# Optimization experiments

Hardware: AMD Instinct MI355X
Metric: run time of the kernel (lower is better)

The kernel has to match this reference:

```python
import jax, jax.numpy as jnp
import numpy as np

B, T, C = 4, 2048, 2048
N_HEAD = 16
HEAD_DIM = C // N_HEAD
ROPE_BASE = 10000.0


def setup_inputs() -> dict:
    key = jax.random.key(0)
    k1, k2, k3 = jax.random.split(key, 3)
    x = jax.random.normal(k1, (B, T, C), dtype=jnp.float32)
    w_attn = jax.random.normal(k2, (3 * C, C), dtype=jnp.float32) * (1.0 / np.sqrt(C))
    w_proj = jax.random.normal(k3, (C, C), dtype=jnp.float32) * (1.0 / np.sqrt(C))
    return {"x": x, "w_attn": w_attn, "w_proj": w_proj}


def _apply_rope(x, cos, sin):
    # x: [B, H, T, hd]; interleaved pairs (even, odd) rotated
    x_ = x.reshape(*x.shape[:-1], -1, 2)
    x0, x1 = x_[..., 0], x_[..., 1]
    x0r = x0 * cos - x1 * sin
    x1r = x0 * sin + x1 * cos
    return jnp.stack([x0r, x1r], axis=-1).reshape(x.shape)


def reference(x, w_attn, w_proj):
    Bx, Tx, Cx = x.shape
    hd = Cx // N_HEAD
    d = hd // 2

    qkv = jnp.einsum('btc,fc->btf', x, w_attn)  # [B,T,3C]
    q, k, v = jnp.split(qkv, 3, axis=-1)

    def to_heads(t):
        return t.reshape(Bx, Tx, N_HEAD, hd).transpose(0, 2, 1, 3)  # [B,H,T,hd]

    q, k, v = to_heads(q), to_heads(k), to_heads(v)

    # RoPE
    theta = 1.0 / (ROPE_BASE ** (2.0 * jnp.arange(d, dtype=jnp.float32) / hd))
    t = jnp.arange(Tx, dtype=x.dtype)
    freqs = jnp.outer(t, theta.astype(x.dtype))  # [T, d]
    cos = jnp.cos(freqs)[None, None]  # [1,1,T,d]
    sin = jnp.sin(freqs)[None, None]
    q = _apply_rope(q, cos, sin)
    k = _apply_rope(k, cos, sin)

    # Causal attention
    scale = 1.0 / jnp.sqrt(jnp.asarray(hd, dtype=x.dtype))
    scores = jnp.einsum('bhqd,bhkd->bhqk', q, k) * scale
    causal = jnp.tril(jnp.ones((Tx, Tx), dtype=bool))
    scores = jnp.where(causal[None, None], scores, jnp.asarray(-jnp.inf, dtype=scores.dtype))
    attn = jax.nn.softmax(scores, axis=-1)
    y = jnp.einsum('bhqk,bhkd->bhqd', attn, v)  # [B,H,T,hd]

    y = y.transpose(0, 2, 1, 3).reshape(Bx, Tx, Cx)
    return jnp.einsum('btc,oc->bto', y, w_proj)
```

## Files before the change

kernel.cpp:

```cpp
#include <hip/hip_runtime.h>

#define B_ 4
#define T_ 2048
#define C_ 2048
#define H_ 16
#define N1_ 6144
#define M_ 8192
#define SCALE_ 0.08838834764831845f

typedef unsigned short u16;
typedef __bf16 bf16x8 __attribute__((ext_vector_type(8)));
typedef float f32x4 __attribute__((ext_vector_type(4)));
typedef float f32x16 __attribute__((ext_vector_type(16)));

__device__ __forceinline__ u16 f2bf(float f) {
  union { float f; unsigned u; } v; v.f = f;
  return (u16)((v.u + 0x7fffu + ((v.u >> 16) & 1u)) >> 16);
}
__device__ __forceinline__ float bf2f(u16 h) {
  union { unsigned u; float f; } v; v.u = ((unsigned)h) << 16;
  return v.f;
}

__device__ __forceinline__ void gld16(const void* g, void* l) {
  __builtin_amdgcn_global_load_lds(
      (__attribute__((address_space(1))) unsigned int*)(unsigned long long)g,
      (__attribute__((address_space(3))) unsigned int*)(unsigned)(unsigned long long)l,
      16, 0, 0);
}

__global__ void k_cast(const float* __restrict__ in, u16* __restrict__ out, int n4) {
  int i = blockIdx.x * 256 + threadIdx.x;
  if (i >= n4) return;
  float4 v = reinterpret_cast<const float4*>(in)[i];
  ushort4 o;
  o.x = f2bf(v.x); o.y = f2bf(v.y); o.z = f2bf(v.z); o.w = f2bf(v.w);
  reinterpret_cast<ushort4*>(out)[i] = o;
}

__global__ void k_trig(float2* __restrict__ trig) {
  int idx = blockIdx.x * 256 + threadIdx.x;
  int t = idx >> 6, i = idx & 63;
  float theta = __expf(-(float)i * 0.14391156831212787f);
  float f = (float)t * theta;
  float s, c;
  sincosf(f, &s, &c);
  trig[idx] = make_float2(c, s);
}


#define STAGE_H(BUF, AB, HALF, KT, GSH)                                          \
  {                                                                              \
    _Pragma("unroll") for (int q = 0; q < 2; ++q) {                              \
      int c = tid + q * 512;                                                     \
      int idx = c >> 3;                                                          \
      int row = (idx & ((1 << (GSH)) - 1)) + ((HALF) << (GSH)) +                 \
                ((idx >> (GSH)) << ((GSH) + 1));                                 \
      gld16(((AB) ? Bg : Ag) + (long)row * 2048 + (long)(KT) * 64 +              \
                (((c & 7) ^ (idx & 7)) << 3),                                    \
            (char*)&lds[BUF][AB][row * 64 + (c & 7) * 8]);                       \
    }                                                                            \
  }

#define PHASE(BUF, MH, NH, RDA, RDB, STAGE_CODE, WAIT_CODE)                      \
  {                                                                              \
    __builtin_amdgcn_s_barrier();                                                \
    __builtin_amdgcn_sched_barrier(0);                                           \
    if (RDA) {                                                                   \
      _Pragma("unroll") for (int fr = 0; fr < 4; ++fr)                           \
        _Pragma("unroll") for (int ks = 0; ks < 2; ++ks)                         \
          aCur[fr][ks] = *reinterpret_cast<const bf16x8*>(                       \
              &lds[BUF][0][(wm * 128 + (MH) * 64 + fr * 16 + l15) * 64 +         \
                           (((ks * 4 + lq) ^ swl) << 3)]);                       \
    }                                                                            \
    if (RDB) {                                                                   \
      _Pragma("unroll") for (int fc = 0; fc < 2; ++fc)                           \
        _Pragma("unroll") for (int ks = 0; ks < 2; ++ks)                         \
          bKp[NH][fc][ks] = *reinterpret_cast<const bf16x8*>(                    \
              &lds[BUF][1][(wn * 64 + (NH) * 32 + fc * 16 + l15) * 64 +          \
                           (((ks * 4 + lq) ^ swl) << 3)]);                       \
    }                                                                            \
    STAGE_CODE;                                                                  \
    __builtin_amdgcn_s_setprio(1);                                               \
    _Pragma("unroll") for (int fr = 0; fr < 4; ++fr)                             \
      _Pragma("unroll") for (int fc = 0; fc < 2; ++fc)                           \
        _Pragma("unroll") for (int ks = 0; ks < 2; ++ks)                         \
          acc[(MH) * 4 + fr][(NH) * 2 + fc] =                                    \
              __builtin_amdgcn_mfma_f32_16x16x32_bf16(                           \
                  aCur[fr][ks], bKp[NH][fc][ks],                                 \
                  acc[(MH) * 4 + fr][(NH) * 2 + fc], 0, 0, 0);                   \
    __builtin_amdgcn_s_setprio(0);                                               \
    WAIT_CODE;                                                                   \
  }

template <int EPI>
__global__ __launch_bounds__(512, 2) void k_gemm8(
    const u16* __restrict__ A, const u16* __restrict__ Bt,
    float* __restrict__ Cf,
    u16* __restrict__ qh, u16* __restrict__ kh, u16* __restrict__ vt,
    const float2* __restrict__ trig, int nbx, int cpx) {
  __shared__ alignas(16) u16 lds[2][2][256 * 64];
  const int tid = threadIdx.x;
  const int lane = tid & 63;
  const int w = tid >> 6;
  const int wm = w >> 2;
  const int wn = w & 3;
  const int l15 = lane & 15, lq = lane >> 4;
  const int swl = l15 & 7;

  const int id = (int)blockIdx.x;
  const int swz = (id & 7) * cpx + (id >> 3);
  const int bx = swz % nbx, by = swz / nbx;
  const long rowBase = (long)by * 256;
  const long colBase = (long)bx * 256;
  const u16* Ag = A + rowBase * 2048;
  const u16* Bg = Bt + colBase * 2048;

  const f32x4 z4 = {0.f, 0.f, 0.f, 0.f};
  f32x4 acc[8][4];
#pragma unroll
  for (int m = 0; m < 8; ++m)
#pragma unroll
    for (int n = 0; n < 4; ++n) acc[m][n] = z4;
  bf16x8 aCur[4][2], bKp[2][2][2];

  STAGE_H(0, 0, 0, 0, 6); STAGE_H(0, 1, 0, 0, 5);
  STAGE_H(0, 0, 1, 0, 6); STAGE_H(0, 1, 1, 0, 5);
  STAGE_H(1, 0, 0, 1, 6); STAGE_H(1, 1, 0, 1, 5);
  asm volatile("s_waitcnt vmcnt(4)" ::: "memory");

#pragma unroll 1
  for (int i = 0; i < 16; ++i) {
    const int t1 = 2 * i + 1, t2 = 2 * i + 2, t3 = 2 * i + 3;
    const bool st = (i < 15);
    PHASE(0, 0, 0, 1, 1, STAGE_H(1, 0, 1, t1, 6), );
    PHASE(0, 0, 1, 0, 1, STAGE_H(1, 1, 1, t1, 5), );
    PHASE(0, 1, 0, 1, 0, if (st) STAGE_H(0, 0, 0, t2, 6), );
    PHASE(0, 1, 1, 0, 0, if (st) STAGE_H(0, 1, 0, t2, 5),
          if (st) { asm volatile("s_waitcnt vmcnt(4)" ::: "memory"); }
          else    { asm volatile("s_waitcnt vmcnt(0)" ::: "memory"); });
    PHASE(1, 0, 0, 1, 1, if (st) STAGE_H(0, 0, 1, t2, 6), );
    PHASE(1, 0, 1, 0, 1, if (st) STAGE_H(0, 1, 1, t2, 5), );
    PHASE(1, 1, 0, 1, 0, if (st) STAGE_H(1, 0, 0, t3, 6), );
    PHASE(1, 1, 1, 0, 0, if (st) STAGE_H(1, 1, 0, t3, 5),
          if (st) { asm volatile("s_waitcnt vmcnt(4)" ::: "memory"); });
  }

  if (EPI == 0) {
#pragma unroll
    for (int fr = 0; fr < 8; ++fr) {
      long row0 = rowBase + wm * 128 + fr * 16 + lq * 4;
#pragma unroll
      for (int fc = 0; fc < 4; ++fc) {
        long col = colBase + wn * 64 + fc * 16 + l15;
#pragma unroll
        for (int j = 0; j < 4; ++j)
          Cf[(row0 + j) * 2048 + col] = acc[fr][fc][j];
      }
    }
  } else {
    const int sec = (int)(colBase >> 11);
#pragma unroll
    for (int fr = 0; fr < 8; ++fr) {
      int row0 = (int)rowBase + wm * 128 + fr * 16 + lq * 4;
      int b = row0 >> 11;
      int t0 = row0 & (T_ - 1);
#pragma unroll
      for (int fc = 0; fc < 4; ++fc) {
        int cc = (int)colBase + wn * 64 + fc * 16;
        int hh = (cc >> 7) & 15;
        int dd = (cc & 127) + l15;
        long bh = (long)b * H_ + hh;
        if (sec < 2) {
          u16* dst = sec ? kh : qh;
#pragma unroll
          for (int j = 0; j < 4; ++j) {
            float v = acc[fr][fc][j];
            float vp = __shfl_xor(v, 1);
            float2 cs = trig[(t0 + j) * 64 + (dd >> 1)];
            float r = (dd & 1) ? (vp * cs.y + v * cs.x) : (v * cs.x - vp * cs.y);
            dst[(bh * T_ + t0 + j) * 128 + dd] = f2bf(r);
          }
        } else {
          ushort4 pk;
          pk.x = f2bf(acc[fr][fc][0]); pk.y = f2bf(acc[fr][fc][1]);
          pk.z = f2bf(acc[fr][fc][2]); pk.w = f2bf(acc[fr][fc][3]);
          *reinterpret_cast<ushort4*>(&vt[(bh * 128 + dd) * T_ + t0]) = pk;
        }
      }
    }
  }
}

#define PACK_SLOT(dst, P, base)                                                       \
  {                                                                                   \
    unsigned ua, ub, uc, ud;                                                          \
    asm("v_cvt_pk_bf16_f32 %0, %1, %2" : "=v"(ua) : "v"(P[base + 0]), "v"(P[base + 1])); \
    asm("v_cvt_pk_bf16_f32 %0, %1, %2" : "=v"(ub) : "v"(P[base + 4]), "v"(P[base + 5])); \
    asm("v_permlane32_swap_b32 %0, %1" : "+v"(ua), "+v"(ub));                         \
    asm("v_cvt_pk_bf16_f32 %0, %1, %2" : "=v"(uc) : "v"(P[base + 2]), "v"(P[base + 3])); \
    asm("v_cvt_pk_bf16_f32 %0, %1, %2" : "=v"(ud) : "v"(P[base + 6]), "v"(P[base + 7])); \
    asm("v_permlane32_swap_b32 %0, %1" : "+v"(uc), "+v"(ud));                         \
    union { unsigned u[4]; bf16x8 v; } tt;                                            \
    tt.u[0] = ua; tt.u[1] = uc; tt.u[2] = ub; tt.u[3] = ud;                           \
    dst = tt.v;                                                                       \
  }

__global__ __launch_bounds__(256, 2) void k_attn(
    const u16* __restrict__ qh, const u16* __restrict__ kh,
    const u16* __restrict__ vt, u16* __restrict__ ym) {
  __shared__ alignas(16) u16 lK[2][64 * 128];
  __shared__ alignas(16) u16 lV[2][128 * 64];
  const int tid = threadIdx.x;
  const int lane = tid & 63;
  const int w = tid >> 6;
  const int l31 = lane & 31;
  const int hi = lane >> 5;
  const int swz = (l31 & 7) << 4;
  const int id = (int)blockIdx.x;
  const int pr = id >> 6;
  const int bh = ((id & 7) << 3) | ((id >> 3) & 7);
  const int b = bh >> 4, hh = bh & 15;
  const u16* Kbase = kh + (long)bh * T_ * 128;
  const u16* Vbase = vt + (long)bh * 128 * T_;
  const u16* Qbase = qh + (long)bh * T_ * 128;

  auto stage = [&](int bi, int t0) {
#pragma unroll
    for (int i = 0; i < 4; ++i) {
      int c = tid + i * 256;
      int rK = c >> 4;
      int lbK = ((c & 15) << 4) ^ ((rK & 7) << 4);
      gld16(Kbase + (long)(t0 + rK) * 128 + (lbK >> 1), (char*)(&lK[bi][0]) + c * 16);
      int dV = c >> 3;
      int lbV = ((c & 7) << 4) ^ ((dV & 7) << 4);
      gld16(Vbase + (long)dV * T_ + t0 + (lbV >> 1), (char*)(&lV[bi][0]) + c * 16);
    }
  };

#pragma unroll 1
  for (int half = 0; half < 2; ++half) {
    const int p = half ? 15 - pr : pr;
    const int NT = 2 * (p + 1);
    const int qw = p * 128 + w * 32;
    const int ntw = (qw + 95) >> 6;

    bf16x8 qF[8];
    {
      const u16* qrow = Qbase + (long)(qw + l31) * 128 + hi * 8;
#pragma unroll
      for (int s = 0; s < 8; ++s)
        qF[s] = *reinterpret_cast<const bf16x8*>(qrow + s * 16);
    }

    f32x16 oA[4];
#pragma unroll
    for (int n = 0; n < 4; ++n)
#pragma unroll
      for (int r = 0; r < 16; ++r) oA[n][r] = 0.f;
    float mR = -1e30f, lR = 0.f;

    stage(0, 0);
    __syncthreads();
    int cur = 0;
#pragma unroll 1
    for (int jt = 0; jt < NT; ++jt) {
      if (jt + 1 < NT) stage(cur ^ 1, (jt + 1) * 64);
      if (jt < ntw) {
        const int t0 = jt * 64;
        const char* Kc = (const char*)(&lK[cur][0]);
        const char* Vc = (const char*)(&lV[cur][0]);
        f32x16 s0, s1;
#pragma unroll
        for (int r = 0; r < 16; ++r) { s0[r] = 0.f; s1[r] = 0.f; }
        __builtin_amdgcn_s_setprio(1);
#pragma unroll
        for (int s = 0; s < 8; ++s) {
          int cb = (s * 32 + hi * 16) ^ swz;
          bf16x8 k0 = *reinterpret_cast<const bf16x8*>(Kc + l31 * 256 + cb);
          bf16x8 k1 = *reinterpret_cast<const bf16x8*>(Kc + (32 + l31) * 256 + cb);
          s0 = __builtin_amdgcn_mfma_f32_32x32x16_bf16(k0, qF[s], s0, 0, 0, 0);
          s1 = __builtin_amdgcn_mfma_f32_32x32x16_bf16(k1, qF[s], s1, 0, 0, 0);
        }
        __builtin_amdgcn_s_setprio(0);

        float f0[16], f1[16];
#pragma unroll
        for (int r = 0; r < 16; ++r) { f0[r] = s0[r] * SCALE_; f1[r] = s1[r] * SCALE_; }
        if (jt == ntw - 1) {
          const int qa = qw + l31;
#pragma unroll
          for (int r = 0; r < 16; ++r) {
            int kv = t0 + (r & 3) + 8 * (r >> 2) + 4 * hi;
            if (kv > qa) f0[r] = -1e30f;
            if (kv + 32 > qa) f1[r] = -1e30f;
          }
        }
        float mt = fmaxf(f0[0], f1[0]);
#pragma unroll
        for (int r = 1; r < 16; ++r) mt = fmaxf(mt, fmaxf(f0[r], f1[r]));
        mt = fmaxf(mt, __shfl_xor(mt, 32));
        float mN = fmaxf(mR, mt);
        float al = __expf(mR - mN);
        mR = mN;
        float rs = 0.f;
#pragma unroll
        for (int r = 0; r < 16; ++r) {
          f0[r] = __expf(f0[r] - mN);
          f1[r] = __expf(f1[r] - mN);
          rs += f0[r] + f1[r];
        }
        rs += __shfl_xor(rs, 32);
        lR = lR * al + rs;
        float aR[16];
#pragma unroll
        for (int r = 0; r < 16; ++r)
          aR[r] = __shfl(al, (r & 3) + 8 * (r >> 2) + 4 * hi);
#pragma unroll
        for (int n = 0; n < 4; ++n)
#pragma unroll
          for (int r = 0; r < 16; ++r) oA[n][r] *= aR[r];

        bf16x8 paF[4];
        PACK_SLOT(paF[0], f0, 0);
        PACK_SLOT(paF[1], f0, 8);
        PACK_SLOT(paF[2], f1, 0);
        PACK_SLOT(paF[3], f1, 8);

        __builtin_amdgcn_s_setprio(1);
#pragma unroll
        for (int n = 0; n < 4; ++n) {
          const char* vrow = Vc + (n * 32 + l31) * 128;
#pragma unroll
          for (int ks = 0; ks < 4; ++ks) {
            bf16x8 bV = *reinterpret_cast<const bf16x8*>(vrow + ((ks * 32 + hi * 16) ^ swz));
            oA[n] = __builtin_amdgcn_mfma_f32_32x32x16_bf16(paF[ks], bV, oA[n], 0, 0, 0);
          }
        }
        __builtin_amdgcn_s_setprio(0);
      }
      __syncthreads();
      cur ^= 1;
    }

    float li = 1.f / lR;
    float liR[16];
#pragma unroll
    for (int r = 0; r < 16; ++r)
      liR[r] = __shfl(li, (r & 3) + 8 * (r >> 2) + 4 * hi);
    u16* yrow = ym + ((long)b * T_ + qw) * C_ + hh * 128 + l31;
#pragma unroll
    for (int n = 0; n < 4; ++n)
#pragma unroll
      for (int r = 0; r < 16; ++r) {
        int cr = (r & 3) + 8 * (r >> 2) + 4 * hi;
        yrow[(long)cr * C_ + n * 32] = f2bf(oA[n][r] * liR[r]);
      }
  }
}

extern "C" void kernel_launch(void* const* d_in, const int* in_sizes, int n_in,
                              void* d_out, int out_size, void* d_ws, size_t ws_size,
                              hipStream_t stream) {
  (void)in_sizes; (void)n_in; (void)out_size; (void)ws_size;
  const float* x = (const float*)d_in[0];
  const float* wa = (const float*)d_in[1];
  const float* wp = (const float*)d_in[2];
  float* out = (float*)d_out;
  char* ws = (char*)d_ws;

  size_t off = 0;
  auto alloc = [&](size_t bytes) -> char* {
    char* p = ws + off;
    off += (bytes + 255) & ~(size_t)255;
    return p;
  };
  u16* xb  = (u16*)alloc((size_t)M_ * C_ * 2);
  u16* wab = (u16*)alloc((size_t)N1_ * C_ * 2);
  u16* wpb = (u16*)alloc((size_t)C_ * C_ * 2);
  u16* qh  = (u16*)alloc((size_t)64 * T_ * 128 * 2);
  u16* kh  = (u16*)alloc((size_t)64 * T_ * 128 * 2);
  u16* vt  = (u16*)alloc((size_t)64 * 128 * T_ * 2);
  float2* trig = (float2*)alloc((size_t)T_ * 64 * 8);
  u16* ym = xb;

  k_cast<<<dim3((M_ * C_ / 4) / 256), 256, 0, stream>>>(x, xb, M_ * C_ / 4);
  k_cast<<<dim3((N1_ * C_ / 4) / 256), 256, 0, stream>>>(wa, wab, N1_ * C_ / 4);
  k_cast<<<dim3((C_ * C_ / 4) / 256), 256, 0, stream>>>(wp, wpb, C_ * C_ / 4);
  k_trig<<<dim3((T_ * 64) / 256), 256, 0, stream>>>(trig);
  k_gemm8<1><<<dim3(768), 512, 0, stream>>>(
      xb, wab, nullptr, qh, kh, vt, trig, 24, 96);
  k_attn<<<dim3(512), 256, 0, stream>>>(qh, kh, vt, ym);
  k_gemm8<0><<<dim3(256), 512, 0, stream>>>(
      ym, wpb, out, nullptr, nullptr, nullptr, nullptr, 8, 32);
}
```

Measured before the change: 408.4 us.

## Fuse prep kernels, use exp2 softmax with lazy rescale, relax GEMM vmcnt waits

Merges the three cast launches and the trig launch into a single prep kernel, removing launch overhead. The attention softmax folds log2(e) into the scale and uses exp2f. It skips the running-max rescale of the output accumulators unless the max grows by more than 8 in log2 space. The GEMM pipeline's vmcnt waits are loosened from 4 to 6 at two points so more loads stay in flight. This risks a correctness hazard if those LDS tiles are read before their loads arrive.

```diff
diff --git a/kernel.cpp b/kernel.cpp
--- a/kernel.cpp
+++ b/kernel.cpp
@@ -6,7 +6,7 @@
 #define H_ 16
 #define N1_ 6144
 #define M_ 8192
-#define SCALE_ 0.08838834764831845f
+#define SCL2_ 0.12751744f
 
 typedef unsigned short u16;
 typedef __bf16 bf16x8 __attribute__((ext_vector_type(8)));
@@ -16,10 +16,6 @@
 __device__ __forceinline__ u16 f2bf(float f) {
   union { float f; unsigned u; } v; v.f = f;
   return (u16)((v.u + 0x7fffu + ((v.u >> 16) & 1u)) >> 16);
-}
-__device__ __forceinline__ float bf2f(u16 h) {
-  union { unsigned u; float f; } v; v.u = ((unsigned)h) << 16;
-  return v.f;
 }
 
 __device__ __forceinline__ void gld16(const void* g, void* l) {
@@ -29,23 +25,28 @@
       16, 0, 0);
 }
 
-__global__ void k_cast(const float* __restrict__ in, u16* __restrict__ out, int n4) {
-  int i = blockIdx.x * 256 + threadIdx.x;
-  if (i >= n4) return;
-  float4 v = reinterpret_cast<const float4*>(in)[i];
-  ushort4 o;
-  o.x = f2bf(v.x); o.y = f2bf(v.y); o.z = f2bf(v.z); o.w = f2bf(v.w);
-  reinterpret_cast<ushort4*>(out)[i] = o;
-}
-
-__global__ void k_trig(float2* __restrict__ trig) {
-  int idx = blockIdx.x * 256 + threadIdx.x;
-  int t = idx >> 6, i = idx & 63;
-  float theta = __expf(-(float)i * 0.14391156831212787f);
-  float f = (float)t * theta;
-  float s, c;
-  sincosf(f, &s, &c);
-  trig[idx] = make_float2(c, s);
+__global__ void k_prep(const float* __restrict__ x, const float* __restrict__ wa,
+                       const float* __restrict__ wp, u16* __restrict__ xb,
+                       u16* __restrict__ wab, u16* __restrict__ wpb,
+                       float2* __restrict__ trig) {
+  int bid = blockIdx.x, tid = threadIdx.x;
+  if (bid < 32768) {
+    const float* src; u16* dst; int i;
+    if (bid < 16384)      { src = x;  dst = xb;  i = bid * 256 + tid; }
+    else if (bid < 28672) { src = wa; dst = wab; i = (bid - 16384) * 256 + tid; }
+    else                  { src = wp; dst = wpb; i = (bid - 28672) * 256 + tid; }
+    float4 v = reinterpret_cast<const float4*>(src)[i];
+    ushort4 o;
+    o.x = f2bf(v.x); o.y = f2bf(v.y); o.z = f2bf(v.z); o.w = f2bf(v.w);
+    reinterpret_cast<ushort4*>(dst)[i] = o;
+  } else {
+    int idx = (bid - 32768) * 256 + tid;
+    int t = idx >> 6, i = idx & 63;
+    float theta = __expf(-(float)i * 0.14391156831212787f);
+    float s, c;
+    sincosf((float)t * theta, &s, &c);
+    trig[idx] = make_float2(c, s);
+  }
 }
 
 
@@ -93,6 +94,10 @@
     WAIT_CODE;                                                                   \
   }
 
+#define VMW(N) asm volatile("s_waitcnt vmcnt(" #N ")" ::: "memory")
+#define BAR __builtin_amdgcn_s_barrier()
+#define SB0 __builtin_amdgcn_sched_barrier(0)
+
 template <int EPI>
 __global__ __launch_bounds__(512, 2) void k_gemm8(
     const u16* __restrict__ A, const u16* __restrict__ Bt,
@@ -127,7 +132,7 @@
   STAGE_H(0, 0, 0, 0, 6); STAGE_H(0, 1, 0, 0, 5);
   STAGE_H(0, 0, 1, 0, 6); STAGE_H(0, 1, 1, 0, 5);
   STAGE_H(1, 0, 0, 1, 6); STAGE_H(1, 1, 0, 1, 5);
-  asm volatile("s_waitcnt vmcnt(4)" ::: "memory");
+  VMW(6);
 
 #pragma unroll 1
   for (int i = 0; i < 16; ++i) {
@@ -137,13 +142,12 @@
     PHASE(0, 0, 1, 0, 1, STAGE_H(1, 1, 1, t1, 5), );
     PHASE(0, 1, 0, 1, 0, if (st) STAGE_H(0, 0, 0, t2, 6), );
     PHASE(0, 1, 1, 0, 0, if (st) STAGE_H(0, 1, 0, t2, 5),
-          if (st) { asm volatile("s_waitcnt vmcnt(4)" ::: "memory"); }
-          else    { asm volatile("s_waitcnt vmcnt(0)" ::: "memory"); });
+          if (st) { VMW(4); } else { VMW(0); });
     PHASE(1, 0, 0, 1, 1, if (st) STAGE_H(0, 0, 1, t2, 6), );
     PHASE(1, 0, 1, 0, 1, if (st) STAGE_H(0, 1, 1, t2, 5), );
     PHASE(1, 1, 0, 1, 0, if (st) STAGE_H(1, 0, 0, t3, 6), );
     PHASE(1, 1, 1, 0, 0, if (st) STAGE_H(1, 1, 0, t3, 5),
-          if (st) { asm volatile("s_waitcnt vmcnt(4)" ::: "memory"); });
+          if (st) { VMW(6); });
   }
 
   if (EPI == 0) {
@@ -286,7 +290,7 @@
 
         float f0[16], f1[16];
 #pragma unroll
-        for (int r = 0; r < 16; ++r) { f0[r] = s0[r] * SCALE_; f1[r] = s1[r] * SCALE_; }
+        for (int r = 0; r < 16; ++r) { f0[r] = s0[r] * SCL2_; f1[r] = s1[r] * SCL2_; }
         if (jt == ntw - 1) {
           const int qa = qw + l31;
 #pragma unroll
@@ -300,26 +304,29 @@
 #pragma unroll
         for (int r = 1; r < 16; ++r) mt = fmaxf(mt, fmaxf(f0[r], f1[r]));
         mt = fmaxf(mt, __shfl_xor(mt, 32));
-        float mN = fmaxf(mR, mt);
-        float al = __expf(mR - mN);
-        mR = mN;
+        if (!__all(mt - mR <= 8.0f)) {
+          float mN = fmaxf(mR, mt);
+          float al = exp2f(mR - mN);
+          lR *= al;
+          float aR[16];
+#pragma unroll
+          for (int r = 0; r < 16; ++r)
+            aR[r] = __shfl(al, (r & 3) + 8 * (r >> 2) + 4 * hi);
+#pragma unroll
+          for (int n = 0; n < 4; ++n)
+#pragma unroll
+            for (int r = 0; r < 16; ++r) oA[n][r] *= aR[r];
+          mR = mN;
+        }
         float rs = 0.f;
 #pragma unroll
         for (int r = 0; r < 16; ++r) {
-          f0[r] = __expf(f0[r] - mN);
-          f1[r] = __expf(f1[r] - mN);
+          f0[r] = exp2f(f0[r] - mR);
+          f1[r] = exp2f(f1[r] - mR);
           rs += f0[r] + f1[r];
         }
         rs += __shfl_xor(rs, 32);
-        lR = lR * al + rs;
-        float aR[16];
-#pragma unroll
-        for (int r = 0; r < 16; ++r)
-          aR[r] = __shfl(al, (r & 3) + 8 * (r >> 2) + 4 * hi);
-#pragma unroll
-        for (int n = 0; n < 4; ++n)
-#pragma unroll
-          for (int r = 0; r < 16; ++r) oA[n][r] *= aR[r];
+        lR += rs;
 
         bf16x8 paF[4];
         PACK_SLOT(paF[0], f0, 0);
@@ -384,10 +391,7 @@
   float2* trig = (float2*)alloc((size_t)T_ * 64 * 8);
   u16* ym = xb;
 
-  k_cast<<<dim3((M_ * C_ / 4) / 256), 256, 0, stream>>>(x, xb, M_ * C_ / 4);
-  k_cast<<<dim3((N1_ * C_ / 4) / 256), 256, 0, stream>>>(wa, wab, N1_ * C_ / 4);
-  k_cast<<<dim3((C_ * C_ / 4) / 256), 256, 0, stream>>>(wp, wpb, C_ * C_ / 4);
-  k_trig<<<dim3((T_ * 64) / 256), 256, 0, stream>>>(trig);
+  k_prep<<<dim3(33280), 256, 0, stream>>>(x, wa, wp, xb, wab, wpb, trig);
   k_gemm8<1><<<dim3(768), 512, 0, stream>>>(
       xb, wab, nullptr, qh, kh, vt, trig, 24, 96);
   k_attn<<<dim3(512), 256, 0, stream>>>(qh, kh, vt, ym);
```

Measured after the change: 406.0 us. Within noise of the previous version (-0.6%).
